# Performance work log

Hardware: AMD Instinct MI355X
Metric: run time of the kernel (lower is better)

Reference implementation:

```python
import jax, jax.numpy as jnp
import numpy as np

B, T, C = 2, 2048, 1024
N_HEAD = 16
HEAD_DIM = C // N_HEAD

def setup_inputs() -> dict:
    key = jax.random.key(0)
    k1, k2, k3 = jax.random.split(key, 3)
    x = jax.random.normal(k1, (B, T, C), dtype=jnp.float32)
    # Dense kernel init scale ~ 1/sqrt(fan_in) for stable softmax
    w_attn = jax.random.normal(k2, (C, 3 * C), dtype=jnp.float32) / np.sqrt(C)
    w_proj = jax.random.normal(k3, (C, C), dtype=jnp.float32) / np.sqrt(C)
    return {"x": x, "w_attn": w_attn, "w_proj": w_proj}

def reference(x, w_attn, w_proj):
    Bc, Tc, Cc = x.shape
    # QKV projection (use_bias=False)
    qkv = x @ w_attn  # [B, T, 3C]
    q, k, v = jnp.split(qkv, 3, axis=-1)
    # [B, T, C] -> [B, H, T, D]
    def heads(a):
        return a.reshape(Bc, Tc, N_HEAD, HEAD_DIM).swapaxes(1, 2)
    q, k, v = heads(q), heads(k), heads(v)
    scale = 1.0 / jnp.sqrt(jnp.asarray(HEAD_DIM, dtype=x.dtype))
    attn = jnp.einsum('bhqd,bhkd->bhqk', q, k) * scale  # [B, H, T, T]
    attn = jax.nn.softmax(attn, axis=-1)
    # dropout=0.0 / deterministic -> identity
    y = jnp.einsum('bhqk,bhkd->bhqd', attn, v)  # [B, H, T, D]
    y = y.swapaxes(1, 2).reshape(Bc, Tc, Cc)
    return y @ w_proj  # output projection, no bias, dropout identity
```

## Files before the change

kernel.cpp:

```cpp
#include <hip/hip_runtime.h>
#include <hip/hip_bf16.h>

#define B_   2
#define T_   2048
#define C_   1024
#define NH_  16
#define HD_  64

typedef __attribute__((ext_vector_type(8))) short short8;
typedef __attribute__((ext_vector_type(4))) float float4_;

static __device__ __forceinline__ unsigned short f2bf(float f) {
    union { float f; unsigned u; } v; v.f = f;
    unsigned r = v.u + 0x7fffu + ((v.u >> 16) & 1u);
    return (unsigned short)(r >> 16);
}

static __device__ __forceinline__ void g2l16(const void* g, void* l) {
    __builtin_amdgcn_global_load_lds(
        (const __attribute__((address_space(1))) void*)g,
        (__attribute__((address_space(3))) void*)l, 16, 0, 0);
}

__global__ __launch_bounds__(256) void conv_bf16(
    const float* __restrict__ in, unsigned short* __restrict__ out, int n8)
{
    int i = blockIdx.x * 256 + threadIdx.x;
    if (i >= n8) return;
    const float4* p = (const float4*)in + (size_t)i * 2;
    float4 a = p[0], b = p[1];
    short8 o;
    o[0]=f2bf(a.x); o[1]=f2bf(a.y); o[2]=f2bf(a.z); o[3]=f2bf(a.w);
    o[4]=f2bf(b.x); o[5]=f2bf(b.y); o[6]=f2bf(b.z); o[7]=f2bf(b.w);
    *((short8*)out + i) = o;
}

__global__ __launch_bounds__(256) void tconv(
    const float* __restrict__ in, unsigned short* __restrict__ out, int R, int Cc)
{
    __shared__ __align__(16) unsigned short Ts[64][72];
    const int t = threadIdx.x;
    const int r0 = blockIdx.x * 64, c0 = blockIdx.y * 64;
    #pragma unroll
    for (int cc = 0; cc < 2; ++cc) {
        int c = t * 2 + cc;
        int r = c >> 3, col = (c & 7) * 8;
        const float* p = in + (size_t)(r0 + r) * Cc + c0 + col;
        #pragma unroll
        for (int i = 0; i < 8; ++i) Ts[col + i][r] = f2bf(p[i]);
    }
    __syncthreads();
    #pragma unroll
    for (int cc = 0; cc < 2; ++cc) {
        int c = t * 2 + cc;
        int cr = c >> 3, oc = (c & 7) * 8;
        uint4 v = *(const uint4*)(&Ts[cr][oc]);
        *(uint4*)(out + (size_t)(c0 + cr) * R + r0 + oc) = v;
    }
}

__global__ __launch_bounds__(256) void vtrans(
    const unsigned short* __restrict__ qkv, unsigned short* __restrict__ vt)
{
    __shared__ __align__(16) unsigned short Ts[64][72];
    const int t = threadIdx.x;
    const int t0 = blockIdx.x * 64, bh = blockIdx.y;
    const int b = bh >> 4, h = bh & 15;
    const unsigned short* Vg = qkv + (size_t)b * T_ * (3 * C_) + 2 * C_ + h * HD_;
    #pragma unroll
    for (int cc = 0; cc < 2; ++cc) {
        int c = t * 2 + cc;
        int r = c >> 3, col = (c & 7) * 8;
        uint4 v = *(const uint4*)(Vg + (size_t)(t0 + r) * (3 * C_) + col);
        const unsigned short* vs = (const unsigned short*)&v;
        #pragma unroll
        for (int i = 0; i < 8; ++i) Ts[col + i][r] = vs[i];
    }
    __syncthreads();
    #pragma unroll
    for (int cc = 0; cc < 2; ++cc) {
        int c = t * 2 + cc;
        int dr = c >> 3, tc = (c & 7) * 8;
        uint4 v = *(const uint4*)(&Ts[dr][tc]);
        *(uint4*)(vt + ((size_t)bh * HD_ + dr) * T_ + t0 + tc) = v;
    }
}

template <bool C_F32>
__global__ __launch_bounds__(256) void gemm_bt(
    const unsigned short* __restrict__ A,
    const unsigned short* __restrict__ Bt,
    void* __restrict__ Cv, int M, int N, int K)
{
    __shared__ __align__(16) unsigned short As[128 * 32];
    __shared__ __align__(16) unsigned short Bs[128 * 32];
    const int t = threadIdx.x, lane = t & 63, w = t >> 6;
    const int quad = lane >> 4, ln = lane & 15;
    const int bm = blockIdx.x, bn = blockIdx.y;
    const int mw = (w & 1) * 64, nw = (w >> 1) * 64;
    float4_ acc[4][4] = {};

    const unsigned short* Ag = A  + (size_t)(bm * 128 + w * 32 + (lane >> 2)) * K + (lane & 3) * 8;
    const unsigned short* Bg = Bt + (size_t)(bn * 128 + w * 32 + (lane >> 2)) * K + (lane & 3) * 8;
    unsigned short* lA = &As[(w * 32) * 32 + lane * 8];
    unsigned short* lB = &Bs[(w * 32) * 32 + lane * 8];

    for (int k0 = 0; k0 < K; k0 += 32) {
        g2l16(Ag + k0,                  lA);
        g2l16(Ag + (size_t)16 * K + k0, lA + 16 * 32);
        g2l16(Bg + k0,                  lB);
        g2l16(Bg + (size_t)16 * K + k0, lB + 16 * 32);
        __syncthreads();
        short8 a[4], b[4];
        #pragma unroll
        for (int i = 0; i < 4; ++i) {
            a[i] = *(const short8*)(&As[(mw + i * 16 + ln) * 32 + quad * 8]);
            b[i] = *(const short8*)(&Bs[(nw + i * 16 + ln) * 32 + quad * 8]);
        }
        #pragma unroll
        for (int mi = 0; mi < 4; ++mi)
            #pragma unroll
            for (int ni = 0; ni < 4; ++ni)
                acc[mi][ni] = __builtin_amdgcn_mfma_f32_16x16x32_bf16(
                    a[mi], b[ni], acc[mi][ni], 0, 0, 0);
        __syncthreads();
    }

    const int row0 = bm * 128 + mw + quad * 4;
    const int col0 = bn * 128 + nw + ln;
    #pragma unroll
    for (int mi = 0; mi < 4; ++mi)
        #pragma unroll
        for (int ni = 0; ni < 4; ++ni)
            #pragma unroll
            for (int i = 0; i < 4; ++i) {
                size_t idx = (size_t)(row0 + mi * 16 + i) * N + col0 + ni * 16;
                if (C_F32) ((float*)Cv)[idx] = acc[mi][ni][i];
                else       ((unsigned short*)Cv)[idx] = f2bf(acc[mi][ni][i]);
            }
}

__global__ __launch_bounds__(256) void attn(
    const unsigned short* __restrict__ qkv,
    const unsigned short* __restrict__ vt,
    unsigned short* __restrict__ Y)
{
    __shared__ __align__(16) unsigned short Qs[64][72];
    __shared__ __align__(16) unsigned short Ks[64][72];
    __shared__ __align__(16) unsigned short Vs[64][72];
    __shared__ __align__(16) unsigned short Ps[64][72];

    const int t = threadIdx.x;
    const int qt = blockIdx.x, bh = blockIdx.y;
    const int b = bh >> 4, h = bh & 15;
    const int lane = t & 63, w = t >> 6;
    const int quad = lane >> 4, ln = lane & 15;

    const unsigned short* Qg  = qkv + (size_t)b * T_ * (3 * C_) + (size_t)h * HD_;
    const unsigned short* Kg  = Qg + C_;
    const unsigned short* Vtg = vt + (size_t)bh * HD_ * T_;

    #pragma unroll
    for (int cc = 0; cc < 2; ++cc) {
        int c = t * 2 + cc;
        int r = c >> 3, col = (c & 7) * 8;
        *(uint4*)(&Qs[r][col]) = *(const uint4*)(Qg + (size_t)(qt * 64 + r) * (3 * C_) + col);
    }
    __syncthreads();

    short8 qf0 = *(const short8*)(&Qs[w * 16 + ln][quad * 8]);
    short8 qf1 = *(const short8*)(&Qs[w * 16 + ln][32 + quad * 8]);

    float4_ o[4] = {};
    float ls[4] = {0.f, 0.f, 0.f, 0.f};
    const float scale = 0.125f;
    const float M0 = 8.0f;

    for (int kt = 0; kt < T_ / 64; ++kt) {
        if (kt) __syncthreads();
        #pragma unroll
        for (int cc = 0; cc < 2; ++cc) {
            int c = t * 2 + cc;
            int r = c >> 3, col = (c & 7) * 8;
            *(uint4*)(&Ks[r][col]) = *(const uint4*)(Kg + (size_t)(kt * 64 + r) * (3 * C_) + col);
            *(uint4*)(&Vs[r][col]) = *(const uint4*)(Vtg + (size_t)r * T_ + kt * 64 + col);
        }
        __syncthreads();

        float4_ s[4] = {};
        #pragma unroll
        for (int ct = 0; ct < 4; ++ct) {
            short8 kb0 = *(const short8*)(&Ks[ct * 16 + ln][quad * 8]);
            short8 kb1 = *(const short8*)(&Ks[ct * 16 + ln][32 + quad * 8]);
            s[ct] = __builtin_amdgcn_mfma_f32_16x16x32_bf16(qf0, kb0, s[ct], 0, 0, 0);
            s[ct] = __builtin_amdgcn_mfma_f32_16x16x32_bf16(qf1, kb1, s[ct], 0, 0, 0);
        }

        #pragma unroll
        for (int ct = 0; ct < 4; ++ct)
            #pragma unroll
            for (int i = 0; i < 4; ++i) {
                float p = __expf(s[ct][i] * scale - M0);
                ls[i] += p;
                Ps[w * 16 + quad * 4 + i][ct * 16 + ln] = f2bf(p);
            }
        __syncthreads();

        short8 pa0 = *(const short8*)(&Ps[w * 16 + ln][quad * 8]);
        short8 pa1 = *(const short8*)(&Ps[w * 16 + ln][32 + quad * 8]);
        #pragma unroll
        for (int dt = 0; dt < 4; ++dt) {
            short8 vb0 = *(const short8*)(&Vs[dt * 16 + ln][quad * 8]);
            short8 vb1 = *(const short8*)(&Vs[dt * 16 + ln][32 + quad * 8]);
            o[dt] = __builtin_amdgcn_mfma_f32_16x16x32_bf16(pa0, vb0, o[dt], 0, 0, 0);
            o[dt] = __builtin_amdgcn_mfma_f32_16x16x32_bf16(pa1, vb1, o[dt], 0, 0, 0);
        }
    }

    #pragma unroll
    for (int off = 1; off < 16; off <<= 1)
        #pragma unroll
        for (int i = 0; i < 4; ++i) ls[i] += __shfl_xor(ls[i], off, 64);

    #pragma unroll
    for (int dt = 0; dt < 4; ++dt)
        #pragma unroll
        for (int i = 0; i < 4; ++i) {
            int row = qt * 64 + w * 16 + quad * 4 + i;
            int col = h * HD_ + dt * 16 + ln;
            Y[((size_t)b * T_ + row) * C_ + col] = f2bf(o[dt][i] / ls[i]);
        }
}

extern "C" void kernel_launch(void* const* d_in, const int* in_sizes, int n_in,
                              void* d_out, int out_size, void* d_ws, size_t ws_size,
                              hipStream_t stream)
{
    const float* x      = (const float*)d_in[0];
    const float* w_attn = (const float*)d_in[1];
    const float* w_proj = (const float*)d_in[2];
    float* out = (float*)d_out;

    unsigned short* qkv = (unsigned short*)d_ws;
    unsigned short* y   = qkv + (size_t)4096 * 3072;
    unsigned short* wTa = y   + (size_t)4096 * 1024;
    unsigned short* wTp = wTa + (size_t)3072 * 1024;
    unsigned short* vt  = wTp + (size_t)1024 * 1024;
    unsigned short* xb  = y;

    conv_bf16<<<2048, 256, 0, stream>>>(x, xb, 4096 * 1024 / 8);
    tconv<<<dim3(16, 48), 256, 0, stream>>>(w_attn, wTa, 1024, 3072);
    tconv<<<dim3(16, 16), 256, 0, stream>>>(w_proj, wTp, 1024, 1024);

    gemm_bt<false><<<dim3(32, 24), 256, 0, stream>>>(xb, wTa, qkv, 4096, 3072, 1024);
    vtrans<<<dim3(32, 32), 256, 0, stream>>>(qkv, vt);
    attn<<<dim3(32, 32), 256, 0, stream>>>(qkv, vt, y);
    gemm_bt<true><<<dim3(32, 8), 256, 0, stream>>>(y, wTp, out, 4096, 1024, 1024);
}
```

Measured before the change: 224.2 us.

## Keep attention probabilities in registers via transposed S and fp16 PV MFMA

The attention kernel computes S transposed (K as the A operand), so the MFMA output layout matches the B operand of a 16x16x16 fp16 MFMA. Probabilities are converted to packed fp16 in registers and fed straight into the P·V product, which removes the Ps shared-memory round trip and one barrier per key tile. Each block now handles 128 queries to reuse K/V tiles, V is transposed into fp16, and the output-projection GEMM uses 64-row tiles to get more blocks. Coalescing indices also change in the transpose kernels. Using fp16 for P and V changes precision, and the unnormalised exp with a fixed max offset could overflow fp16 for larger scores.

Result: slower. 229.5 us (+2.4%).

```diff
diff --git a/kernel.cpp b/kernel.cpp
--- a/kernel.cpp
+++ b/kernel.cpp
@@ -9,11 +9,17 @@
 
 typedef __attribute__((ext_vector_type(8))) short short8;
 typedef __attribute__((ext_vector_type(4))) float float4_;
+typedef __attribute__((ext_vector_type(4))) _Float16 half4_;
+typedef __attribute__((ext_vector_type(2))) __fp16  fp16x2;
 
 static __device__ __forceinline__ unsigned short f2bf(float f) {
     union { float f; unsigned u; } v; v.f = f;
     unsigned r = v.u + 0x7fffu + ((v.u >> 16) & 1u);
     return (unsigned short)(r >> 16);
+}
+static __device__ __forceinline__ float bf2f(unsigned short b) {
+    union { unsigned u; float f; } v; v.u = (unsigned)b << 16;
+    return v.f;
 }
 
 static __device__ __forceinline__ void g2l16(const void* g, void* l) {
@@ -43,7 +49,7 @@
     const int r0 = blockIdx.x * 64, c0 = blockIdx.y * 64;
     #pragma unroll
     for (int cc = 0; cc < 2; ++cc) {
-        int c = t * 2 + cc;
+        int c = cc * 256 + t;
         int r = c >> 3, col = (c & 7) * 8;
         const float* p = in + (size_t)(r0 + r) * Cc + c0 + col;
         #pragma unroll
@@ -52,7 +58,7 @@
     __syncthreads();
     #pragma unroll
     for (int cc = 0; cc < 2; ++cc) {
-        int c = t * 2 + cc;
+        int c = cc * 256 + t;
         int cr = c >> 3, oc = (c & 7) * 8;
         uint4 v = *(const uint4*)(&Ts[cr][oc]);
         *(uint4*)(out + (size_t)(c0 + cr) * R + r0 + oc) = v;
@@ -69,69 +75,77 @@
     const unsigned short* Vg = qkv + (size_t)b * T_ * (3 * C_) + 2 * C_ + h * HD_;
     #pragma unroll
     for (int cc = 0; cc < 2; ++cc) {
-        int c = t * 2 + cc;
+        int c = cc * 256 + t;
         int r = c >> 3, col = (c & 7) * 8;
         uint4 v = *(const uint4*)(Vg + (size_t)(t0 + r) * (3 * C_) + col);
         const unsigned short* vs = (const unsigned short*)&v;
         #pragma unroll
-        for (int i = 0; i < 8; ++i) Ts[col + i][r] = vs[i];
+        for (int i = 0; i < 8; ++i) {
+            union { __fp16 h; unsigned short u; } cv;
+            cv.h = (__fp16)bf2f(vs[i]);
+            Ts[col + i][r] = cv.u;
+        }
     }
     __syncthreads();
     #pragma unroll
     for (int cc = 0; cc < 2; ++cc) {
-        int c = t * 2 + cc;
+        int c = cc * 256 + t;
         int dr = c >> 3, tc = (c & 7) * 8;
         uint4 v = *(const uint4*)(&Ts[dr][tc]);
         *(uint4*)(vt + ((size_t)bh * HD_ + dr) * T_ + t0 + tc) = v;
     }
 }
 
-template <bool C_F32>
+template <bool C_F32, int BM>
 __global__ __launch_bounds__(256) void gemm_bt(
     const unsigned short* __restrict__ A,
     const unsigned short* __restrict__ Bt,
     void* __restrict__ Cv, int M, int N, int K)
 {
-    __shared__ __align__(16) unsigned short As[128 * 32];
+    __shared__ __align__(16) unsigned short As[BM * 32];
     __shared__ __align__(16) unsigned short Bs[128 * 32];
     const int t = threadIdx.x, lane = t & 63, w = t >> 6;
     const int quad = lane >> 4, ln = lane & 15;
     const int bm = blockIdx.x, bn = blockIdx.y;
-    const int mw = (w & 1) * 64, nw = (w >> 1) * 64;
-    float4_ acc[4][4] = {};
-
-    const unsigned short* Ag = A  + (size_t)(bm * 128 + w * 32 + (lane >> 2)) * K + (lane & 3) * 8;
+    constexpr int NI = (BM == 128) ? 4 : 2;
+    const int mw = (BM == 128) ? (w & 1) * 64 : 0;
+    const int nw = (BM == 128) ? (w >> 1) * 64 : w * 32;
+    float4_ acc[4][NI] = {};
+
+    constexpr int AROWS = BM / 4;
+    const unsigned short* Ag = A  + (size_t)(bm * BM + w * AROWS + (lane >> 2)) * K + (lane & 3) * 8;
     const unsigned short* Bg = Bt + (size_t)(bn * 128 + w * 32 + (lane >> 2)) * K + (lane & 3) * 8;
-    unsigned short* lA = &As[(w * 32) * 32 + lane * 8];
+    unsigned short* lA = &As[(w * AROWS) * 32 + lane * 8];
     unsigned short* lB = &Bs[(w * 32) * 32 + lane * 8];
 
     for (int k0 = 0; k0 < K; k0 += 32) {
-        g2l16(Ag + k0,                  lA);
-        g2l16(Ag + (size_t)16 * K + k0, lA + 16 * 32);
+        g2l16(Ag + k0, lA);
+        if (BM == 128) g2l16(Ag + (size_t)16 * K + k0, lA + 16 * 32);
         g2l16(Bg + k0,                  lB);
         g2l16(Bg + (size_t)16 * K + k0, lB + 16 * 32);
         __syncthreads();
-        short8 a[4], b[4];
-        #pragma unroll
-        for (int i = 0; i < 4; ++i) {
+        short8 a[4], b[NI];
+        #pragma unroll
+        for (int i = 0; i < 4; ++i)
             a[i] = *(const short8*)(&As[(mw + i * 16 + ln) * 32 + quad * 8]);
+        #pragma unroll
+        for (int i = 0; i < NI; ++i)
             b[i] = *(const short8*)(&Bs[(nw + i * 16 + ln) * 32 + quad * 8]);
-        }
         #pragma unroll
         for (int mi = 0; mi < 4; ++mi)
             #pragma unroll
-            for (int ni = 0; ni < 4; ++ni)
+            for (int ni = 0; ni < NI; ++ni)
                 acc[mi][ni] = __builtin_amdgcn_mfma_f32_16x16x32_bf16(
                     a[mi], b[ni], acc[mi][ni], 0, 0, 0);
         __syncthreads();
     }
 
-    const int row0 = bm * 128 + mw + quad * 4;
+    const int row0 = bm * BM + mw + quad * 4;
     const int col0 = bn * 128 + nw + ln;
     #pragma unroll
     for (int mi = 0; mi < 4; ++mi)
         #pragma unroll
-        for (int ni = 0; ni < 4; ++ni)
+        for (int ni = 0; ni < NI; ++ni)
             #pragma unroll
             for (int i = 0; i < 4; ++i) {
                 size_t idx = (size_t)(row0 + mi * 16 + i) * N + col0 + ni * 16;
@@ -145,10 +159,9 @@
     const unsigned short* __restrict__ vt,
     unsigned short* __restrict__ Y)
 {
-    __shared__ __align__(16) unsigned short Qs[64][72];
+    __shared__ __align__(16) unsigned short Qs[128][72];
     __shared__ __align__(16) unsigned short Ks[64][72];
     __shared__ __align__(16) unsigned short Vs[64][72];
-    __shared__ __align__(16) unsigned short Ps[64][72];
 
     const int t = threadIdx.x;
     const int qt = blockIdx.x, bh = blockIdx.y;
@@ -161,18 +174,22 @@
     const unsigned short* Vtg = vt + (size_t)bh * HD_ * T_;
 
     #pragma unroll
-    for (int cc = 0; cc < 2; ++cc) {
-        int c = t * 2 + cc;
+    for (int cc = 0; cc < 4; ++cc) {
+        int c = cc * 256 + t;
         int r = c >> 3, col = (c & 7) * 8;
-        *(uint4*)(&Qs[r][col]) = *(const uint4*)(Qg + (size_t)(qt * 64 + r) * (3 * C_) + col);
+        *(uint4*)(&Qs[r][col]) = *(const uint4*)(Qg + (size_t)(qt * 128 + r) * (3 * C_) + col);
     }
     __syncthreads();
 
-    short8 qf0 = *(const short8*)(&Qs[w * 16 + ln][quad * 8]);
-    short8 qf1 = *(const short8*)(&Qs[w * 16 + ln][32 + quad * 8]);
-
-    float4_ o[4] = {};
-    float ls[4] = {0.f, 0.f, 0.f, 0.f};
+    short8 qf[2][2];
+    #pragma unroll
+    for (int qm = 0; qm < 2; ++qm)
+        #pragma unroll
+        for (int dh = 0; dh < 2; ++dh)
+            qf[qm][dh] = *(const short8*)(&Qs[w * 32 + qm * 16 + ln][dh * 32 + quad * 8]);
+
+    float4_ ot[4][2] = {};
+    float ls[2] = {0.f, 0.f};
     const float scale = 0.125f;
     const float M0 = 8.0f;
 
@@ -180,56 +197,69 @@
         if (kt) __syncthreads();
         #pragma unroll
         for (int cc = 0; cc < 2; ++cc) {
-            int c = t * 2 + cc;
+            int c = cc * 256 + t;
             int r = c >> 3, col = (c & 7) * 8;
             *(uint4*)(&Ks[r][col]) = *(const uint4*)(Kg + (size_t)(kt * 64 + r) * (3 * C_) + col);
             *(uint4*)(&Vs[r][col]) = *(const uint4*)(Vtg + (size_t)r * T_ + kt * 64 + col);
         }
         __syncthreads();
 
-        float4_ s[4] = {};
-        #pragma unroll
-        for (int ct = 0; ct < 4; ++ct) {
-            short8 kb0 = *(const short8*)(&Ks[ct * 16 + ln][quad * 8]);
-            short8 kb1 = *(const short8*)(&Ks[ct * 16 + ln][32 + quad * 8]);
-            s[ct] = __builtin_amdgcn_mfma_f32_16x16x32_bf16(qf0, kb0, s[ct], 0, 0, 0);
-            s[ct] = __builtin_amdgcn_mfma_f32_16x16x32_bf16(qf1, kb1, s[ct], 0, 0, 0);
-        }
-
+        float4_ st[4][2] = {};
         #pragma unroll
         for (int ct = 0; ct < 4; ++ct)
             #pragma unroll
-            for (int i = 0; i < 4; ++i) {
-                float p = __expf(s[ct][i] * scale - M0);
-                ls[i] += p;
-                Ps[w * 16 + quad * 4 + i][ct * 16 + ln] = f2bf(p);
-            }
-        __syncthreads();
-
-        short8 pa0 = *(const short8*)(&Ps[w * 16 + ln][quad * 8]);
-        short8 pa1 = *(const short8*)(&Ps[w * 16 + ln][32 + quad * 8]);
-        #pragma unroll
-        for (int dt = 0; dt < 4; ++dt) {
-            short8 vb0 = *(const short8*)(&Vs[dt * 16 + ln][quad * 8]);
-            short8 vb1 = *(const short8*)(&Vs[dt * 16 + ln][32 + quad * 8]);
-            o[dt] = __builtin_amdgcn_mfma_f32_16x16x32_bf16(pa0, vb0, o[dt], 0, 0, 0);
-            o[dt] = __builtin_amdgcn_mfma_f32_16x16x32_bf16(pa1, vb1, o[dt], 0, 0, 0);
-        }
-    }
-
-    #pragma unroll
-    for (int off = 1; off < 16; off <<= 1)
-        #pragma unroll
-        for (int i = 0; i < 4; ++i) ls[i] += __shfl_xor(ls[i], off, 64);
-
-    #pragma unroll
-    for (int dt = 0; dt < 4; ++dt)
-        #pragma unroll
-        for (int i = 0; i < 4; ++i) {
-            int row = qt * 64 + w * 16 + quad * 4 + i;
-            int col = h * HD_ + dt * 16 + ln;
-            Y[((size_t)b * T_ + row) * C_ + col] = f2bf(o[dt][i] / ls[i]);
-        }
+            for (int dh = 0; dh < 2; ++dh) {
+                short8 kb = *(const short8*)(&Ks[ct * 16 + ln][dh * 32 + quad * 8]);
+                #pragma unroll
+                for (int qm = 0; qm < 2; ++qm)
+                    st[ct][qm] = __builtin_amdgcn_mfma_f32_16x16x32_bf16(
+                        kb, qf[qm][dh], st[ct][qm], 0, 0, 0);
+            }
+
+        half4_ pf[4][2];
+        #pragma unroll
+        for (int ct = 0; ct < 4; ++ct)
+            #pragma unroll
+            for (int qm = 0; qm < 2; ++qm) {
+                float p0 = __expf(st[ct][qm][0] * scale - M0);
+                float p1 = __expf(st[ct][qm][1] * scale - M0);
+                float p2 = __expf(st[ct][qm][2] * scale - M0);
+                float p3 = __expf(st[ct][qm][3] * scale - M0);
+                ls[qm] += (p0 + p1) + (p2 + p3);
+                union { fp16x2 h2[2]; half4_ h4; } u;
+                u.h2[0] = __builtin_amdgcn_cvt_pkrtz(p0, p1);
+                u.h2[1] = __builtin_amdgcn_cvt_pkrtz(p2, p3);
+                pf[ct][qm] = u.h4;
+            }
+
+        #pragma unroll
+        for (int dt = 0; dt < 4; ++dt)
+            #pragma unroll
+            for (int ct = 0; ct < 4; ++ct) {
+                half4_ va = *(const half4_*)(&Vs[dt * 16 + ln][ct * 16 + quad * 4]);
+                #pragma unroll
+                for (int qm = 0; qm < 2; ++qm)
+                    ot[dt][qm] = __builtin_amdgcn_mfma_f32_16x16x16f16(
+                        va, pf[ct][qm], ot[dt][qm], 0, 0, 0);
+            }
+    }
+
+    #pragma unroll
+    for (int qm = 0; qm < 2; ++qm) {
+        ls[qm] += __shfl_xor(ls[qm], 16, 64);
+        ls[qm] += __shfl_xor(ls[qm], 32, 64);
+    }
+
+    #pragma unroll
+    for (int qm = 0; qm < 2; ++qm) {
+        unsigned short* Yr = Y + ((size_t)b * T_ + qt * 128 + w * 32 + qm * 16 + ln) * C_ + h * HD_;
+        float inv = 1.0f / ls[qm];
+        #pragma unroll
+        for (int dt = 0; dt < 4; ++dt)
+            #pragma unroll
+            for (int i = 0; i < 4; ++i)
+                Yr[dt * 16 + quad * 4 + i] = f2bf(ot[dt][qm][i] * inv);
+    }
 }
 
 extern "C" void kernel_launch(void* const* d_in, const int* in_sizes, int n_in,
@@ -252,8 +282,8 @@
     tconv<<<dim3(16, 48), 256, 0, stream>>>(w_attn, wTa, 1024, 3072);
     tconv<<<dim3(16, 16), 256, 0, stream>>>(w_proj, wTp, 1024, 1024);
 
-    gemm_bt<false><<<dim3(32, 24), 256, 0, stream>>>(xb, wTa, qkv, 4096, 3072, 1024);
+    gemm_bt<false, 128><<<dim3(32, 24), 256, 0, stream>>>(xb, wTa, qkv, 4096, 3072, 1024);
     vtrans<<<dim3(32, 32), 256, 0, stream>>>(qkv, vt);
-    attn<<<dim3(32, 32), 256, 0, stream>>>(qkv, vt, y);
-    gemm_bt<true><<<dim3(32, 8), 256, 0, stream>>>(y, wTp, out, 4096, 1024, 1024);
-}
+    attn<<<dim3(16, 32), 256, 0, stream>>>(qkv, vt, y);
+    gemm_bt<true, 64><<<dim3(64, 8), 256, 0, stream>>>(y, wTp, out, 4096, 1024, 1024);
+}
```
